# Kernel optimization log

Hardware: AMD Instinct MI355X
Metric: run time of the kernel (lower is better)

## Reference

```python
import jax, jax.numpy as jnp
import numpy as np

B, N, T, DM, H, M = 32, 207, 24, 64, 8, 32
E = 2 * DM  # true input feature dim (2*dmodel per the reshape in the source)


def setup_inputs() -> dict:
    rng = jax.random.key(0)
    ks = jax.random.split(rng, 10)
    s = 0.05  # scale params to keep activations numerically sane
    query = jax.random.normal(ks[0], (B, N, T, E), jnp.float32)
    key = jax.random.normal(ks[1], (B, N, T, E), jnp.float32)
    value = jax.random.normal(ks[2], (B, N, T, E), jnp.float32)
    # causal temporal mask, broadcast over batch/node/head; True = masked out
    atten_mask = jnp.broadcast_to(jnp.triu(jnp.ones((T, T), bool), 1), (B, N, 1, T, T))
    qp1 = jax.random.normal(ks[3], (N * DM, M), jnp.float32) * s
    qp2 = jax.random.normal(ks[4], (M, 4 * DM), jnp.float32) * s
    kp1 = jax.random.normal(ks[5], (N * DM, M), jnp.float32) * s
    kp2 = jax.random.normal(ks[6], (M, 4 * DM), jnp.float32) * s
    vp1 = jax.random.normal(ks[7], (N * DM, M), jnp.float32) * s
    vp2 = jax.random.normal(ks[8], (M, 4 * DM), jnp.float32) * s
    out_W = jax.random.normal(ks[9], (E, DM), jnp.float32) * s
    out_b = jnp.zeros((DM,), jnp.float32)
    return dict(query=query, key=key, value=value, atten_mask=atten_mask,
                qp1=qp1, qp2=qp2, kp1=kp1, kp2=kp2, vp1=vp1, vp2=vp2,
                out_W=out_W, out_b=out_b, num_heads=H)


def reference(query, key, value, atten_mask, qp1, qp2, kp1, kp2, vp1, vp2, out_W, out_b, num_heads):
    b, n, t, e = query.shape

    def proj(x, p1, p2):
        # low-rank factored per-node projection: (N*dmodel, M) @ (M, 4*dmodel) -> (N, E, E)
        P = (p1 @ p2).reshape(n, e, e)
        y = jnp.einsum('bnti,nik->bntk', x, P)
        return jax.nn.relu(y).reshape(b, n, t, num_heads, -1)

    q = proj(query, qp1, qp2)   # (B,N,T,H,d)
    k = proj(key, kp1, kp2)
    v = proj(value, vp1, vp2)

    scale = 1.0 / np.sqrt(q.shape[-1]).astype(np.float32)
    scores = jnp.einsum('bnthe,bnshe->bnhts', q, k)          # (B,N,H,T,S)
    scores = jnp.where(atten_mask, -jnp.inf, scores)          # masked_fill before scaling
    attn = jax.nn.softmax(scale * scores, axis=-1)            # dropout disabled (eval)
    out = jnp.einsum('bnhts,bnshd->bnthd', attn, v).reshape(b, n, t, -1)
    out = jax.nn.relu(out @ out_W + out_b)                    # (B,N,T,dmodel)
    return out, attn
```

## Files before the change

### kernel.cpp

```cpp
#include <hip/hip_runtime.h>
#include <hip/hip_bf16.h>

#define Bn 32
#define Nn 207
#define Tt 24
#define Ee 128
#define Hh 8
#define Dm 64
#define Mm 32

typedef __attribute__((ext_vector_type(8))) short bf16x8;
typedef __attribute__((ext_vector_type(4))) float f32x4;

__device__ __forceinline__ unsigned swz256(unsigned a) { return a ^ (((a >> 8) & 7u) << 4); }
__device__ __forceinline__ unsigned swz64(unsigned a)  { return a ^ (((a >> 7) & 3u) << 4); }
__device__ __forceinline__ unsigned short f2b(float f) {
  union { float f; unsigned u; } x; x.f = f;
  unsigned u = x.u;
  return (unsigned short)((u + 0x7FFFu + ((u >> 16) & 1u)) >> 16);
}

__global__ __launch_bounds__(256) void build_P_frag(const float* __restrict__ p1,
                                                    const float* __restrict__ p2,
                                                    unsigned short* __restrict__ Pt) {
  const int bid = blockIdx.x;
  const int n = bid >> 3;
  const int r8 = bid & 7;
  const int ks = r8 >> 1;
  const int chunk = ((r8 & 1) << 1) + (threadIdx.x >> 7);
  const int col = threadIdx.x & 127;
  const int base_i = ks * 32 + chunk * 8;
  const float* p1r = p1 + (size_t)(n * 64 + (base_i >> 1)) * Mm;
  const float* p2a = p2 + col;
  const float* p2b = p2 + 128 + col;
  float acc[8] = {};
#pragma unroll
  for (int m = 0; m < Mm; ++m) {
    float a = p2a[m * 256], b = p2b[m * 256];
#pragma unroll
    for (int jj = 0; jj < 4; ++jj) {
      float pv = p1r[jj * Mm + m];
      acc[2 * jj]     = fmaf(pv, a, acc[2 * jj]);
      acc[2 * jj + 1] = fmaf(pv, b, acc[2 * jj + 1]);
    }
  }
  const int nt = col >> 4;
  const int lane = (chunk << 4) | (col & 15);
  union { unsigned short u[8]; uint4 v; } w;
#pragma unroll
  for (int j = 0; j < 8; ++j) w.u[j] = f2b(acc[j]);
  *(uint4*)(Pt + (size_t)(((n * 8 + nt) * 4 + ks) * 64 + lane) * 8) = w.v;
}

__global__ __launch_bounds__(256) void build_W_frag(const float* __restrict__ W,
                                                    unsigned short* __restrict__ Wt) {
  for (int idx = threadIdx.x; idx < 1024; idx += 256) {
    int lane = idx & 63, ks = (idx >> 6) & 3, nt = idx >> 8;
    union { unsigned short u[8]; uint4 v; } w;
#pragma unroll
    for (int j = 0; j < 8; ++j)
      w.u[j] = f2b(W[(size_t)(ks * 32 + (lane >> 4) * 8 + j) * 64 + nt * 16 + (lane & 15)]);
    *(uint4*)(Wt + (size_t)idx * 8) = w.v;
  }
}

__global__ __launch_bounds__(256, 3) void fused_attn(
    const float* __restrict__ Qin, const float* __restrict__ Kin,
    const float* __restrict__ Vin,
    const unsigned short* __restrict__ Ptq, const unsigned short* __restrict__ Ptk,
    const unsigned short* __restrict__ Ptv, const unsigned short* __restrict__ Wt,
    const float* __restrict__ bias,
    float* __restrict__ out, float* __restrict__ attn) {
  __shared__ __align__(16) char smem[49152];
  const int tid = threadIdx.x;
  const int lane = tid & 63;
  const int wv = tid >> 6;
  const int c = lane & 15;
  const int g = lane >> 4;
  const f32x4 zf = {0.f, 0.f, 0.f, 0.f};

  int bx = blockIdx.x;
  bx = (bx & 7) * 828 + (bx >> 3);
  const int n = bx >> 5;
  const int b = bx & 31;
  const size_t xbase = (size_t)(b * Nn + n) * (Tt * Ee);

  {
    uint4 z4 = {0, 0, 0, 0};
#pragma unroll
    for (int i = 0; i < 2; ++i) *(uint4*)(smem + 24576 + (tid + 256 * i) * 16) = z4;
    const float* src[2] = {Qin + xbase, Kin + xbase};
#pragma unroll
    for (int w = 0; w < 2; ++w)
#pragma unroll
      for (int it = 0; it < 3; ++it) {
        int e4 = tid + 256 * it;
        float4 xv = *(const float4*)(src[w] + (size_t)e4 * 4);
        unsigned a = swz256((e4 >> 5) * 256 + (e4 & 31) * 8);
        uint2 pk;
        pk.x = (unsigned)f2b(xv.x) | ((unsigned)f2b(xv.y) << 16);
        pk.y = (unsigned)f2b(xv.z) | ((unsigned)f2b(xv.w) << 16);
        *(uint2*)(smem + w * 8192 + a) = pk;
      }
  }
  __syncthreads();

#pragma unroll
  for (int w = 0; w < 2; ++w) {
    const unsigned short* Pt = (w == 0) ? Ptq : Ptk;
    f32x4 acc[2][2] = {{zf, zf}, {zf, zf}};
#pragma unroll
    for (int ks = 0; ks < 4; ++ks) {
      bf16x8 Bf[2], Af[2];
#pragma unroll
      for (int ntl = 0; ntl < 2; ++ntl)
        Bf[ntl] = *(const bf16x8*)(Pt + (size_t)(((n * 8 + (wv * 2 + ntl)) * 4 + ks) * 64 + lane) * 8);
#pragma unroll
      for (int mt = 0; mt < 2; ++mt)
        Af[mt] = *(const bf16x8*)(smem + w * 8192 + swz256((mt * 16 + c) * 256 + ks * 64 + g * 16));
#pragma unroll
      for (int mt = 0; mt < 2; ++mt)
#pragma unroll
        for (int ntl = 0; ntl < 2; ++ntl)
          acc[mt][ntl] = __builtin_amdgcn_mfma_f32_16x16x32_bf16(Af[mt], Bf[ntl], acc[mt][ntl], 0, 0, 0);
    }
    char* dst = smem + ((w == 0) ? 32768 : 16384);
#pragma unroll
    for (int mt = 0; mt < 2; ++mt)
#pragma unroll
      for (int r = 0; r < 4; ++r) {
        int row = mt * 16 + g * 4 + r;
        if (row < 24) {
#pragma unroll
          for (int ntl = 0; ntl < 2; ++ntl) {
            int col = (wv * 2 + ntl) * 16 + c;
            *(unsigned short*)(dst + swz256(row * 256 + col * 2)) = f2b(fmaxf(acc[mt][ntl][r], 0.f));
          }
        }
      }
  }

  float4 xvr[3];
#pragma unroll
  for (int it = 0; it < 3; ++it)
    xvr[it] = *(const float4*)(Vin + xbase + (size_t)(tid + 256 * it) * 4);
  __syncthreads();

  f32x4 sc[2][2][2];
  {
    bf16x8 zb = {0, 0, 0, 0, 0, 0, 0, 0};
#pragma unroll
    for (int hh = 0; hh < 2; ++hh) {
      int h = wv * 2 + hh;
      bf16x8 Aq[2], Bk[2];
#pragma unroll
      for (int mt = 0; mt < 2; ++mt) {
        Aq[mt] = zb;
        if (lane < 32)
          Aq[mt] = *(const bf16x8*)(smem + 32768 + swz256((mt * 16 + c) * 256 + (h * 16 + g * 8) * 2));
      }
#pragma unroll
      for (int st = 0; st < 2; ++st) {
        Bk[st] = zb;
        if (lane < 32)
          Bk[st] = *(const bf16x8*)(smem + 16384 + swz256((st * 16 + c) * 256 + (h * 16 + g * 8) * 2));
      }
#pragma unroll
      for (int mt = 0; mt < 2; ++mt)
#pragma unroll
        for (int st = 0; st < 2; ++st)
          sc[hh][mt][st] = __builtin_amdgcn_mfma_f32_16x16x32_bf16(Aq[mt], Bk[st], zf, 0, 0, 0);
    }
  }
  __syncthreads();

#pragma unroll
  for (int it = 0; it < 3; ++it) {
    int e4 = tid + 256 * it;
    unsigned a = swz256((e4 >> 5) * 256 + (e4 & 31) * 8);
    uint2 pk;
    pk.x = (unsigned)f2b(xvr[it].x) | ((unsigned)f2b(xvr[it].y) << 16);
    pk.y = (unsigned)f2b(xvr[it].z) | ((unsigned)f2b(xvr[it].w) << 16);
    *(uint2*)(smem + a) = pk;
  }

  {
    const size_t abase = (size_t)(b * Nn + n) * (Hh * Tt * Tt);
#pragma unroll
    for (int hh = 0; hh < 2; ++hh) {
      int h = wv * 2 + hh;
#pragma unroll
      for (int mt = 0; mt < 2; ++mt)
#pragma unroll
        for (int r = 0; r < 4; ++r) {
          int t = mt * 16 + g * 4 + r;
          float v0 = (c <= t)      ? sc[hh][mt][0][r] * 0.25f : -1e30f;
          float v1 = (16 + c <= t) ? sc[hh][mt][1][r] * 0.25f : -1e30f;
          float m = fmaxf(v0, v1);
          m = fmaxf(m, __shfl_xor(m, 1));
          m = fmaxf(m, __shfl_xor(m, 2));
          m = fmaxf(m, __shfl_xor(m, 4));
          m = fmaxf(m, __shfl_xor(m, 8));
          float e0 = __expf(v0 - m);
          float e1 = __expf(v1 - m);
          float s2 = e0 + e1;
          s2 += __shfl_xor(s2, 1);
          s2 += __shfl_xor(s2, 2);
          s2 += __shfl_xor(s2, 4);
          s2 += __shfl_xor(s2, 8);
          float inv = 1.0f / s2;
          float p0 = e0 * inv, p1 = e1 * inv;
          if (t < 24) {
            float* ap = attn + abase + (size_t)h * (Tt * Tt) + t * Tt;
            ap[c] = p0;
            if (c < 8) ap[16 + c] = p1;
            char* q = smem + 32768;
            *(unsigned short*)(q + swz64(h * 2048 + t * 64 + c * 2))        = f2b(p0);
            *(unsigned short*)(q + swz64(h * 2048 + t * 64 + (16 + c) * 2)) = f2b(p1);
          }
        }
    }
  }
  __syncthreads();

  {
    f32x4 acc[2][2] = {{zf, zf}, {zf, zf}};
#pragma unroll
    for (int ks = 0; ks < 4; ++ks) {
      bf16x8 Bf[2], Af[2];
#pragma unroll
      for (int ntl = 0; ntl < 2; ++ntl)
        Bf[ntl] = *(const bf16x8*)(Ptv + (size_t)(((n * 8 + (wv * 2 + ntl)) * 4 + ks) * 64 + lane) * 8);
#pragma unroll
      for (int mt = 0; mt < 2; ++mt)
        Af[mt] = *(const bf16x8*)(smem + swz256((mt * 16 + c) * 256 + ks * 64 + g * 16));
#pragma unroll
      for (int mt = 0; mt < 2; ++mt)
#pragma unroll
        for (int ntl = 0; ntl < 2; ++ntl)
          acc[mt][ntl] = __builtin_amdgcn_mfma_f32_16x16x32_bf16(Af[mt], Bf[ntl], acc[mt][ntl], 0, 0, 0);
    }
#pragma unroll
    for (int mt = 0; mt < 2; ++mt)
#pragma unroll
      for (int r = 0; r < 4; ++r) {
        int srow = mt * 16 + g * 4 + r;
        if (srow < 24) {
#pragma unroll
          for (int ntl = 0; ntl < 2; ++ntl) {
            int dcol = (wv * 2 + ntl) * 16 + c;
            *(unsigned short*)(smem + 24576 + swz64(dcol * 64 + srow * 2)) = f2b(fmaxf(acc[mt][ntl][r], 0.f));
          }
        }
      }
  }
  __syncthreads();

  {
    f32x4 pv[2][2];
#pragma unroll
    for (int hh = 0; hh < 2; ++hh) {
      int h = wv * 2 + hh;
      bf16x8 Bv = *(const bf16x8*)(smem + 24576 + swz64((h * 16 + c) * 64 + g * 16));
#pragma unroll
      for (int mt = 0; mt < 2; ++mt) {
        bf16x8 Ap = *(const bf16x8*)(smem + 32768 + swz64(h * 2048 + (mt * 16 + c) * 64 + g * 16));
        pv[hh][mt] = __builtin_amdgcn_mfma_f32_16x16x32_bf16(Ap, Bv, zf, 0, 0, 0);
      }
    }
#pragma unroll
    for (int hh = 0; hh < 2; ++hh) {
      int h = wv * 2 + hh;
#pragma unroll
      for (int mt = 0; mt < 2; ++mt)
#pragma unroll
        for (int r = 0; r < 4; ++r) {
          int t = mt * 16 + g * 4 + r;
          if (t < 24)
            *(unsigned short*)(smem + 8192 + swz256(t * 256 + (h * 16 + c) * 2)) = f2b(pv[hh][mt][r]);
        }
    }
  }
  __syncthreads();

  {
    f32x4 acc[2] = {zf, zf};
#pragma unroll
    for (int ks = 0; ks < 4; ++ks) {
      bf16x8 Bw = *(const bf16x8*)(Wt + (size_t)((wv * 4 + ks) * 64 + lane) * 8);
      bf16x8 Af[2];
#pragma unroll
      for (int mt = 0; mt < 2; ++mt)
        Af[mt] = *(const bf16x8*)(smem + 8192 + swz256((mt * 16 + c) * 256 + ks * 64 + g * 16));
#pragma unroll
      for (int mt = 0; mt < 2; ++mt)
        acc[mt] = __builtin_amdgcn_mfma_f32_16x16x32_bf16(Af[mt], Bw, acc[mt], 0, 0, 0);
    }
    int j = wv * 16 + c;
    float bj = bias[j];
    const size_t obase = (size_t)(b * Nn + n) * (Tt * Dm);
#pragma unroll
    for (int mt = 0; mt < 2; ++mt)
#pragma unroll
      for (int r = 0; r < 4; ++r) {
        int t = mt * 16 + g * 4 + r;
        if (t < 24) out[obase + (size_t)t * Dm + j] = fmaxf(acc[mt][r] + bj, 0.f);
      }
  }
}

extern "C" void kernel_launch(void* const* d_in, const int* in_sizes, int n_in,
                              void* d_out, int out_size, void* d_ws, size_t ws_size,
                              hipStream_t stream) {
  const float* query = (const float*)d_in[0];
  const float* key   = (const float*)d_in[1];
  const float* value = (const float*)d_in[2];
  const float* qp1 = (const float*)d_in[4];
  const float* qp2 = (const float*)d_in[5];
  const float* kp1 = (const float*)d_in[6];
  const float* kp2 = (const float*)d_in[7];
  const float* vp1 = (const float*)d_in[8];
  const float* vp2 = (const float*)d_in[9];
  const float* out_W = (const float*)d_in[10];
  const float* out_b = (const float*)d_in[11];

  const size_t PT = (size_t)Nn * 8 * 4 * 64 * 8;
  unsigned short* Ptq = (unsigned short*)d_ws;
  unsigned short* Ptk = Ptq + PT;
  unsigned short* Ptv = Ptk + PT;
  unsigned short* Wtf = Ptv + PT;

  float* out = (float*)d_out;
  float* attn = out + (size_t)Bn * Nn * Tt * Dm;

  build_P_frag<<<Nn * 8, 256, 0, stream>>>(qp1, qp2, Ptq);
  build_P_frag<<<Nn * 8, 256, 0, stream>>>(kp1, kp2, Ptk);
  build_P_frag<<<Nn * 8, 256, 0, stream>>>(vp1, vp2, Ptv);
  build_W_frag<<<1, 256, 0, stream>>>(out_W, Wtf);

  fused_attn<<<Bn * Nn, 256, 0, stream>>>(query, key, value, Ptq, Ptk, Ptv, Wtf,
                                          out_b, out, attn);
}
```

Before: 186.1 us.

## Split fused attention into batched projection GEMM and separate attention kernel

Result: slower. 229.1 us (+23.1%).

```diff
diff --git a/kernel.cpp b/kernel.cpp
--- a/kernel.cpp
+++ b/kernel.cpp
@@ -8,21 +8,29 @@
 #define Hh 8
 #define Dm 64
 #define Mm 32
+#define NBN (Bn * Nn)
+#define PT ((size_t)Nn * 16384)
 
 typedef __attribute__((ext_vector_type(8))) short bf16x8;
 typedef __attribute__((ext_vector_type(4))) float f32x4;
 
 __device__ __forceinline__ unsigned swz256(unsigned a) { return a ^ (((a >> 8) & 7u) << 4); }
 __device__ __forceinline__ unsigned swz64(unsigned a)  { return a ^ (((a >> 7) & 3u) << 4); }
-__device__ __forceinline__ unsigned short f2b(float f) {
+__device__ __forceinline__ unsigned f2b(float f) {
   union { float f; unsigned u; } x; x.f = f;
   unsigned u = x.u;
-  return (unsigned short)((u + 0x7FFFu + ((u >> 16) & 1u)) >> 16);
-}
-
-__global__ __launch_bounds__(256) void build_P_frag(const float* __restrict__ p1,
-                                                    const float* __restrict__ p2,
-                                                    unsigned short* __restrict__ Pt) {
+  return ((u + 0x7FFFu + ((u >> 16) & 1u)) >> 16) & 0xFFFFu;
+}
+
+__global__ __launch_bounds__(256) void build_P_frag3(
+    const float* __restrict__ qp1, const float* __restrict__ qp2,
+    const float* __restrict__ kp1, const float* __restrict__ kp2,
+    const float* __restrict__ vp1, const float* __restrict__ vp2,
+    unsigned short* __restrict__ Pt) {
+  const int tau = blockIdx.y;
+  const float* p1 = (tau == 0) ? qp1 : (tau == 1) ? kp1 : vp1;
+  const float* p2 = (tau == 0) ? qp2 : (tau == 1) ? kp2 : vp2;
+  unsigned short* dst = Pt + (size_t)tau * PT;
   const int bid = blockIdx.x;
   const int n = bid >> 3;
   const int r8 = bid & 7;
@@ -48,8 +56,8 @@
   const int lane = (chunk << 4) | (col & 15);
   union { unsigned short u[8]; uint4 v; } w;
 #pragma unroll
-  for (int j = 0; j < 8; ++j) w.u[j] = f2b(acc[j]);
-  *(uint4*)(Pt + (size_t)(((n * 8 + nt) * 4 + ks) * 64 + lane) * 8) = w.v;
+  for (int j = 0; j < 8; ++j) w.u[j] = (unsigned short)f2b(acc[j]);
+  *(uint4*)(dst + (size_t)(((n * 8 + nt) * 4 + ks) * 64 + lane) * 8) = w.v;
 }
 
 __global__ __launch_bounds__(256) void build_W_frag(const float* __restrict__ W,
@@ -59,133 +67,126 @@
     union { unsigned short u[8]; uint4 v; } w;
 #pragma unroll
     for (int j = 0; j < 8; ++j)
-      w.u[j] = f2b(W[(size_t)(ks * 32 + (lane >> 4) * 8 + j) * 64 + nt * 16 + (lane & 15)]);
+      w.u[j] = (unsigned short)f2b(W[(size_t)(ks * 32 + (lane >> 4) * 8 + j) * 64 + nt * 16 + (lane & 15)]);
     *(uint4*)(Wt + (size_t)idx * 8) = w.v;
   }
 }
 
-__global__ __launch_bounds__(256, 3) void fused_attn(
-    const float* __restrict__ Qin, const float* __restrict__ Kin,
-    const float* __restrict__ Vin,
-    const unsigned short* __restrict__ Ptq, const unsigned short* __restrict__ Ptk,
-    const unsigned short* __restrict__ Ptv, const unsigned short* __restrict__ Wt,
+__global__ __launch_bounds__(384) void proj_gemm(
+    const float* __restrict__ Xq, const float* __restrict__ Xk, const float* __restrict__ Xv,
+    const unsigned short* __restrict__ Pt,
+    unsigned short* __restrict__ Qw, unsigned short* __restrict__ Kw,
+    unsigned short* __restrict__ Vw) {
+  __shared__ __align__(16) char smem[24576];
+  const int tau = blockIdx.y;
+  const float* X = (tau == 0) ? Xq : (tau == 1) ? Xk : Xv;
+  const unsigned short* Pf = Pt + (size_t)tau * PT;
+  int gbl = blockIdx.x;
+  int bx = (gbl & 7) * 207 + (gbl >> 3);
+  const int n = bx >> 3, bt = bx & 7;
+  const int b0 = bt * 4;
+  const int tid = threadIdx.x;
+
+#pragma unroll
+  for (int b_rel = 0; b_rel < 4; ++b_rel) {
+    const float* src = X + ((size_t)(b0 + b_rel) * Nn + n) * (Tt * Ee);
+#pragma unroll
+    for (int i = 0; i < 2; ++i) {
+      int idx = tid + 384 * i;
+      float4 xv = *(const float4*)(src + (size_t)idx * 4);
+      unsigned a = swz256((unsigned)((b_rel * 24 + (idx >> 5)) * 256 + (idx & 31) * 8));
+      uint2 pk;
+      pk.x = f2b(xv.x) | (f2b(xv.y) << 16);
+      pk.y = f2b(xv.z) | (f2b(xv.w) << 16);
+      *(uint2*)(smem + a) = pk;
+    }
+  }
+  __syncthreads();
+
+  const int w = tid >> 6, lane = tid & 63, c = lane & 15, g = lane >> 4;
+  const f32x4 zf = {0.f, 0.f, 0.f, 0.f};
+  f32x4 acc[8] = {zf, zf, zf, zf, zf, zf, zf, zf};
+#pragma unroll
+  for (int ks = 0; ks < 4; ++ks) {
+    bf16x8 Af = *(const bf16x8*)(smem + swz256((unsigned)((w * 16 + c) * 256 + ks * 64 + g * 16)));
+#pragma unroll
+    for (int ntl = 0; ntl < 8; ++ntl) {
+      bf16x8 Bf = *(const bf16x8*)(Pf + (size_t)(((n * 8 + ntl) * 4 + ks) * 64 + lane) * 8);
+      acc[ntl] = __builtin_amdgcn_mfma_f32_16x16x32_bf16(Af, Bf, acc[ntl], 0, 0, 0);
+    }
+  }
+
+  if (tau < 2) {
+    unsigned short* Yw = (tau == 0) ? Qw : Kw;
+#pragma unroll
+    for (int r = 0; r < 4; ++r) {
+      int m = w * 16 + g * 4 + r;
+      int b_rel = m / 24, t = m - b_rel * 24;
+      size_t rowb = (((size_t)(b0 + b_rel) * Nn + n) * Tt + t) * Ee;
+#pragma unroll
+      for (int ntl = 0; ntl < 8; ++ntl)
+        Yw[rowb + ntl * 16 + c] = (unsigned short)f2b(fmaxf(acc[ntl][r], 0.f));
+    }
+  } else {
+#pragma unroll
+    for (int r = 0; r < 4; ++r) {
+      int m = w * 16 + g * 4 + r;
+      int b_rel = m / 24, t = m - b_rel * 24;
+      size_t tb = ((size_t)(b0 + b_rel) * Nn + n) * 4096;
+#pragma unroll
+      for (int ntl = 0; ntl < 8; ++ntl)
+        Vw[tb + (size_t)(ntl * 16 + c) * 32 + t] = (unsigned short)f2b(fmaxf(acc[ntl][r], 0.f));
+    }
+    for (int idx = tid; idx < 512; idx += 384) {
+      int b_rel = idx >> 7, e = idx & 127;
+      uint4 z = {0, 0, 0, 0};
+      *(uint4*)(Vw + ((size_t)(b0 + b_rel) * Nn + n) * 4096 + (size_t)e * 32 + 24) = z;
+    }
+  }
+}
+
+__global__ __launch_bounds__(256) void attn_k2(
+    const unsigned short* __restrict__ Qw, const unsigned short* __restrict__ Kw,
+    const unsigned short* __restrict__ Vw, const unsigned short* __restrict__ Wt,
     const float* __restrict__ bias,
     float* __restrict__ out, float* __restrict__ attn) {
-  __shared__ __align__(16) char smem[49152];
+  __shared__ __align__(16) char smem[24576];
   const int tid = threadIdx.x;
   const int lane = tid & 63;
   const int wv = tid >> 6;
   const int c = lane & 15;
   const int g = lane >> 4;
   const f32x4 zf = {0.f, 0.f, 0.f, 0.f};
-
-  int bx = blockIdx.x;
-  bx = (bx & 7) * 828 + (bx >> 3);
-  const int n = bx >> 5;
-  const int b = bx & 31;
-  const size_t xbase = (size_t)(b * Nn + n) * (Tt * Ee);
+  const bf16x8 zb = {0, 0, 0, 0, 0, 0, 0, 0};
+  const int bn = blockIdx.x;
+  const unsigned short* qb = Qw + (size_t)bn * 3072;
+  const unsigned short* kb = Kw + (size_t)bn * 3072;
+  const unsigned short* vb = Vw + (size_t)bn * 4096;
+
+  f32x4 sc[2][2][2];
+#pragma unroll
+  for (int hh = 0; hh < 2; ++hh) {
+    int h = wv * 2 + hh;
+    bf16x8 Aq[2], Bk[2];
+#pragma unroll
+    for (int mt = 0; mt < 2; ++mt) {
+      Aq[mt] = zb;
+      if (lane < 32) Aq[mt] = *(const bf16x8*)(qb + (size_t)(mt * 16 + c) * Ee + h * 16 + g * 8);
+    }
+#pragma unroll
+    for (int st = 0; st < 2; ++st) {
+      Bk[st] = zb;
+      if (lane < 32) Bk[st] = *(const bf16x8*)(kb + (size_t)(st * 16 + c) * Ee + h * 16 + g * 8);
+    }
+#pragma unroll
+    for (int mt = 0; mt < 2; ++mt)
+#pragma unroll
+      for (int st = 0; st < 2; ++st)
+        sc[hh][mt][st] = __builtin_amdgcn_mfma_f32_16x16x32_bf16(Aq[mt], Bk[st], zf, 0, 0, 0);
+  }
 
   {
-    uint4 z4 = {0, 0, 0, 0};
-#pragma unroll
-    for (int i = 0; i < 2; ++i) *(uint4*)(smem + 24576 + (tid + 256 * i) * 16) = z4;
-    const float* src[2] = {Qin + xbase, Kin + xbase};
-#pragma unroll
-    for (int w = 0; w < 2; ++w)
-#pragma unroll
-      for (int it = 0; it < 3; ++it) {
-        int e4 = tid + 256 * it;
-        float4 xv = *(const float4*)(src[w] + (size_t)e4 * 4);
-        unsigned a = swz256((e4 >> 5) * 256 + (e4 & 31) * 8);
-        uint2 pk;
-        pk.x = (unsigned)f2b(xv.x) | ((unsigned)f2b(xv.y) << 16);
-        pk.y = (unsigned)f2b(xv.z) | ((unsigned)f2b(xv.w) << 16);
-        *(uint2*)(smem + w * 8192 + a) = pk;
-      }
-  }
-  __syncthreads();
-
-#pragma unroll
-  for (int w = 0; w < 2; ++w) {
-    const unsigned short* Pt = (w == 0) ? Ptq : Ptk;
-    f32x4 acc[2][2] = {{zf, zf}, {zf, zf}};
-#pragma unroll
-    for (int ks = 0; ks < 4; ++ks) {
-      bf16x8 Bf[2], Af[2];
-#pragma unroll
-      for (int ntl = 0; ntl < 2; ++ntl)
-        Bf[ntl] = *(const bf16x8*)(Pt + (size_t)(((n * 8 + (wv * 2 + ntl)) * 4 + ks) * 64 + lane) * 8);
-#pragma unroll
-      for (int mt = 0; mt < 2; ++mt)
-        Af[mt] = *(const bf16x8*)(smem + w * 8192 + swz256((mt * 16 + c) * 256 + ks * 64 + g * 16));
-#pragma unroll
-      for (int mt = 0; mt < 2; ++mt)
-#pragma unroll
-        for (int ntl = 0; ntl < 2; ++ntl)
-          acc[mt][ntl] = __builtin_amdgcn_mfma_f32_16x16x32_bf16(Af[mt], Bf[ntl], acc[mt][ntl], 0, 0, 0);
-    }
-    char* dst = smem + ((w == 0) ? 32768 : 16384);
-#pragma unroll
-    for (int mt = 0; mt < 2; ++mt)
-#pragma unroll
-      for (int r = 0; r < 4; ++r) {
-        int row = mt * 16 + g * 4 + r;
-        if (row < 24) {
-#pragma unroll
-          for (int ntl = 0; ntl < 2; ++ntl) {
-            int col = (wv * 2 + ntl) * 16 + c;
-            *(unsigned short*)(dst + swz256(row * 256 + col * 2)) = f2b(fmaxf(acc[mt][ntl][r], 0.f));
-          }
-        }
-      }
-  }
-
-  float4 xvr[3];
-#pragma unroll
-  for (int it = 0; it < 3; ++it)
-    xvr[it] = *(const float4*)(Vin + xbase + (size_t)(tid + 256 * it) * 4);
-  __syncthreads();
-
-  f32x4 sc[2][2][2];
-  {
-    bf16x8 zb = {0, 0, 0, 0, 0, 0, 0, 0};
-#pragma unroll
-    for (int hh = 0; hh < 2; ++hh) {
-      int h = wv * 2 + hh;
-      bf16x8 Aq[2], Bk[2];
-#pragma unroll
-      for (int mt = 0; mt < 2; ++mt) {
-        Aq[mt] = zb;
-        if (lane < 32)
-          Aq[mt] = *(const bf16x8*)(smem + 32768 + swz256((mt * 16 + c) * 256 + (h * 16 + g * 8) * 2));
-      }
-#pragma unroll
-      for (int st = 0; st < 2; ++st) {
-        Bk[st] = zb;
-        if (lane < 32)
-          Bk[st] = *(const bf16x8*)(smem + 16384 + swz256((st * 16 + c) * 256 + (h * 16 + g * 8) * 2));
-      }
-#pragma unroll
-      for (int mt = 0; mt < 2; ++mt)
-#pragma unroll
-        for (int st = 0; st < 2; ++st)
-          sc[hh][mt][st] = __builtin_amdgcn_mfma_f32_16x16x32_bf16(Aq[mt], Bk[st], zf, 0, 0, 0);
-    }
-  }
-  __syncthreads();
-
-#pragma unroll
-  for (int it = 0; it < 3; ++it) {
-    int e4 = tid + 256 * it;
-    unsigned a = swz256((e4 >> 5) * 256 + (e4 & 31) * 8);
-    uint2 pk;
-    pk.x = (unsigned)f2b(xvr[it].x) | ((unsigned)f2b(xvr[it].y) << 16);
-    pk.y = (unsigned)f2b(xvr[it].z) | ((unsigned)f2b(xvr[it].w) << 16);
-    *(uint2*)(smem + a) = pk;
-  }
-
-  {
-    const size_t abase = (size_t)(b * Nn + n) * (Hh * Tt * Tt);
+    const size_t abase = (size_t)bn * (Hh * Tt * Tt);
 #pragma unroll
     for (int hh = 0; hh < 2; ++hh) {
       int h = wv * 2 + hh;
@@ -214,9 +215,8 @@
             float* ap = attn + abase + (size_t)h * (Tt * Tt) + t * Tt;
             ap[c] = p0;
             if (c < 8) ap[16 + c] = p1;
-            char* q = smem + 32768;
-            *(unsigned short*)(q + swz64(h * 2048 + t * 64 + c * 2))        = f2b(p0);
-            *(unsigned short*)(q + swz64(h * 2048 + t * 64 + (16 + c) * 2)) = f2b(p1);
+            *(unsigned short*)(smem + swz64((unsigned)(h * 2048 + t * 64 + c * 2)))        = (unsigned short)f2b(p0);
+            *(unsigned short*)(smem + swz64((unsigned)(h * 2048 + t * 64 + (16 + c) * 2))) = (unsigned short)f2b(p1);
           }
         }
     }
@@ -224,47 +224,14 @@
   __syncthreads();
 
   {
-    f32x4 acc[2][2] = {{zf, zf}, {zf, zf}};
-#pragma unroll
-    for (int ks = 0; ks < 4; ++ks) {
-      bf16x8 Bf[2], Af[2];
-#pragma unroll
-      for (int ntl = 0; ntl < 2; ++ntl)
-        Bf[ntl] = *(const bf16x8*)(Ptv + (size_t)(((n * 8 + (wv * 2 + ntl)) * 4 + ks) * 64 + lane) * 8);
-#pragma unroll
-      for (int mt = 0; mt < 2; ++mt)
-        Af[mt] = *(const bf16x8*)(smem + swz256((mt * 16 + c) * 256 + ks * 64 + g * 16));
-#pragma unroll
-      for (int mt = 0; mt < 2; ++mt)
-#pragma unroll
-        for (int ntl = 0; ntl < 2; ++ntl)
-          acc[mt][ntl] = __builtin_amdgcn_mfma_f32_16x16x32_bf16(Af[mt], Bf[ntl], acc[mt][ntl], 0, 0, 0);
-    }
-#pragma unroll
-    for (int mt = 0; mt < 2; ++mt)
-#pragma unroll
-      for (int r = 0; r < 4; ++r) {
-        int srow = mt * 16 + g * 4 + r;
-        if (srow < 24) {
-#pragma unroll
-          for (int ntl = 0; ntl < 2; ++ntl) {
-            int dcol = (wv * 2 + ntl) * 16 + c;
-            *(unsigned short*)(smem + 24576 + swz64(dcol * 64 + srow * 2)) = f2b(fmaxf(acc[mt][ntl][r], 0.f));
-          }
-        }
-      }
-  }
-  __syncthreads();
-
-  {
     f32x4 pv[2][2];
 #pragma unroll
     for (int hh = 0; hh < 2; ++hh) {
       int h = wv * 2 + hh;
-      bf16x8 Bv = *(const bf16x8*)(smem + 24576 + swz64((h * 16 + c) * 64 + g * 16));
+      bf16x8 Bv = *(const bf16x8*)(vb + (size_t)(h * 16 + c) * 32 + g * 8);
 #pragma unroll
       for (int mt = 0; mt < 2; ++mt) {
-        bf16x8 Ap = *(const bf16x8*)(smem + 32768 + swz64(h * 2048 + (mt * 16 + c) * 64 + g * 16));
+        bf16x8 Ap = *(const bf16x8*)(smem + swz64((unsigned)(h * 2048 + (mt * 16 + c) * 64 + g * 16)));
         pv[hh][mt] = __builtin_amdgcn_mfma_f32_16x16x32_bf16(Ap, Bv, zf, 0, 0, 0);
       }
     }
@@ -277,34 +244,33 @@
         for (int r = 0; r < 4; ++r) {
           int t = mt * 16 + g * 4 + r;
           if (t < 24)
-            *(unsigned short*)(smem + 8192 + swz256(t * 256 + (h * 16 + c) * 2)) = f2b(pv[hh][mt][r]);
+            *(unsigned short*)(smem + 16384 + swz256((unsigned)(t * 256 + (h * 16 + c) * 2))) =
+                (unsigned short)f2b(pv[hh][mt][r]);
         }
     }
   }
   __syncthreads();
 
   {
-    f32x4 acc[2] = {zf, zf};
+    f32x4 acc2[2] = {zf, zf};
 #pragma unroll
     for (int ks = 0; ks < 4; ++ks) {
       bf16x8 Bw = *(const bf16x8*)(Wt + (size_t)((wv * 4 + ks) * 64 + lane) * 8);
-      bf16x8 Af[2];
-#pragma unroll
-      for (int mt = 0; mt < 2; ++mt)
-        Af[mt] = *(const bf16x8*)(smem + 8192 + swz256((mt * 16 + c) * 256 + ks * 64 + g * 16));
-#pragma unroll
-      for (int mt = 0; mt < 2; ++mt)
-        acc[mt] = __builtin_amdgcn_mfma_f32_16x16x32_bf16(Af[mt], Bw, acc[mt], 0, 0, 0);
+#pragma unroll
+      for (int mt = 0; mt < 2; ++mt) {
+        bf16x8 Af = *(const bf16x8*)(smem + 16384 + swz256((unsigned)((mt * 16 + c) * 256 + ks * 64 + g * 16)));
+        acc2[mt] = __builtin_amdgcn_mfma_f32_16x16x32_bf16(Af, Bw, acc2[mt], 0, 0, 0);
+      }
     }
     int j = wv * 16 + c;
     float bj = bias[j];
-    const size_t obase = (size_t)(b * Nn + n) * (Tt * Dm);
+    const size_t obase = (size_t)bn * (Tt * Dm);
 #pragma unroll
     for (int mt = 0; mt < 2; ++mt)
 #pragma unroll
       for (int r = 0; r < 4; ++r) {
         int t = mt * 16 + g * 4 + r;
-        if (t < 24) out[obase + (size_t)t * Dm + j] = fmaxf(acc[mt][r] + bj, 0.f);
+        if (t < 24) out[obase + (size_t)t * Dm + j] = fmaxf(acc2[mt][r] + bj, 0.f);
       }
   }
 }
@@ -324,20 +290,17 @@
   const float* out_W = (const float*)d_in[10];
   const float* out_b = (const float*)d_in[11];
 
-  const size_t PT = (size_t)Nn * 8 * 4 * 64 * 8;
-  unsigned short* Ptq = (unsigned short*)d_ws;
-  unsigned short* Ptk = Ptq + PT;
-  unsigned short* Ptv = Ptk + PT;
-  unsigned short* Wtf = Ptv + PT;
+  unsigned short* Pt  = (unsigned short*)d_ws;
+  unsigned short* Wtf = Pt + 3 * PT;
+  unsigned short* Qw  = Wtf + 8192;
+  unsigned short* Kw  = Qw + (size_t)NBN * 3072;
+  unsigned short* Vw  = Kw + (size_t)NBN * 3072;
 
   float* out = (float*)d_out;
-  float* attn = out + (size_t)Bn * Nn * Tt * Dm;
-
-  build_P_frag<<<Nn * 8, 256, 0, stream>>>(qp1, qp2, Ptq);
-  build_P_frag<<<Nn * 8, 256, 0, stream>>>(kp1, kp2, Ptk);
-  build_P_frag<<<Nn * 8, 256, 0, stream>>>(vp1, vp2, Ptv);
+  float* attn = out + (size_t)NBN * Tt * Dm;
+
+  build_P_frag3<<<dim3(Nn * 8, 3), 256, 0, stream>>>(qp1, qp2, kp1, kp2, vp1, vp2, Pt);
   build_W_frag<<<1, 256, 0, stream>>>(out_W, Wtf);
-
-  fused_attn<<<Bn * Nn, 256, 0, stream>>>(query, key, value, Ptq, Ptk, Ptv, Wtf,
-                                          out_b, out, attn);
-}
+  proj_gemm<<<dim3(1656, 3), 384, 0, stream>>>(query, key, value, Pt, Qw, Kw, Vw);
+  attn_k2<<<NBN, 256, 0, stream>>>(Qw, Kw, Vw, Wtf, out_b, out, attn);
+}
```
